# Performance work log

Hardware: AMD Instinct MI355X
Metric: run time of the kernel (lower is better)

The kernel has to match this reference:

```python
import jax, jax.numpy as jnp
import numpy as np
from jax import lax

H = 2048      # d_inner
N = 8         # half of d_state (conjugate-pair complex modes)
B, L, D_MODEL = 4, 4096, 1024
D_CONV = 4


def setup_inputs() -> dict:
    key = jax.random.key(0)
    ks = jax.random.split(key, 10)
    hidden_states = jax.random.normal(ks[0], (B, L, D_MODEL), dtype=jnp.float32)
    W_in = jax.random.normal(ks[1], (2 * H, D_MODEL), dtype=jnp.float32) / np.sqrt(D_MODEL)
    conv_w = jax.random.normal(ks[2], (H, D_CONV), dtype=jnp.float32) / np.sqrt(D_CONV)
    conv_b = jax.random.normal(ks[3], (H,), dtype=jnp.float32) * 0.1
    # S4D params: dt ~ loguniform(1e-3, 1e-1); A = -0.5 + i*pi*n (legs-ish diag init)
    u = jax.random.uniform(ks[4], (H,), dtype=jnp.float32)
    log_dt = jnp.log(1e-3) + u * (jnp.log(1e-1) - jnp.log(1e-3))
    log_A_real = jnp.log(0.5 * jnp.ones((H, N), dtype=jnp.float32))
    A_imag = jnp.pi * jnp.broadcast_to(jnp.arange(N, dtype=jnp.float32), (H, N)).copy()
    C_re = jax.random.normal(ks[5], (H, N), dtype=jnp.float32)
    C_im = jax.random.normal(ks[6], (H, N), dtype=jnp.float32)
    D = jnp.ones((H,), dtype=jnp.float32)
    W_out = jax.random.normal(ks[7], (D_MODEL, H), dtype=jnp.float32) / np.sqrt(H)
    return dict(hidden_states=hidden_states, W_in=W_in, conv_w=conv_w, conv_b=conv_b,
                log_dt=log_dt, log_A_real=log_A_real, A_imag=A_imag,
                C_re=C_re, C_im=C_im, D=D, W_out=W_out)


def _s4d_kernel(log_dt, log_A_real, A_imag, C_re, C_im, L):
    # S4D (diagonal SSM) convolution kernel, ZOH-style discretization.
    dt = jnp.exp(log_dt)                       # (H,)
    A = -jnp.exp(log_A_real) + 1j * A_imag      # (H,N) complex
    C = C_re + 1j * C_im                        # (H,N)
    dtA = dt[:, None] * A                       # (H,N)
    Ct = C * (jnp.exp(dtA) - 1.0) / A           # (H,N)
    t = jnp.arange(L, dtype=jnp.float32)
    vand = jnp.exp(dtA[:, :, None] * t)         # (H,N,L) Vandermonde
    return 2.0 * jnp.einsum('hn,hnl->hl', Ct, vand).real  # (H,L)


def reference(hidden_states, W_in, conv_w, conv_b, log_dt, log_A_real, A_imag, C_re, C_im, D, W_out):
    B, L, _ = hidden_states.shape
    # in_proj (no bias): (B,L,D) -> (B, 2H, L)
    xz = jnp.einsum('bld,ed->bel', hidden_states, W_in)
    x, z = jnp.split(xz, 2, axis=1)             # each (B,H,L)
    # causal depthwise conv1d + SiLU
    w = conv_w.shape[-1]
    xp = jnp.pad(x, ((0, 0), (0, 0), (w - 1, 0)))
    x = lax.conv_general_dilated(xp, conv_w[:, None, :], (1,), 'VALID',
                                 dimension_numbers=('NCH', 'OIH', 'NCH'),
                                 feature_group_count=x.shape[1])
    x = jax.nn.silu(x + conv_b[None, :, None])
    # S4 FFT long convolution + D skip
    k = _s4d_kernel(log_dt, log_A_real, A_imag, C_re, C_im, L)  # (H,L)
    n = 2 * L
    y = jnp.fft.irfft(jnp.fft.rfft(x, n=n) * jnp.fft.rfft(k, n=n), n=n)[..., :L]
    y = y + x * D[None, :, None]
    # SiLU gate and out_proj
    y = y * jax.nn.silu(z)
    return jnp.einsum('bhl,dh->bld', y, W_out)
```

## Files before the change

kernel.cpp:

```cpp
#include <hip/hip_runtime.h>
#include <hip/hip_bf16.h>
#include <math.h>

#define H_DIM 2048
#define N_ST 8
#define B_SZ 4
#define L_SEQ 4096
#define DMODEL 1024
#define DCONV 4
#define CL 128
#define NC (L_SEQ / CL)

typedef __bf16 bf16x8 __attribute__((ext_vector_type(8)));
typedef __bf16 bf16x4 __attribute__((ext_vector_type(4)));
typedef float f32x4 __attribute__((ext_vector_type(4)));

typedef const unsigned int __attribute__((address_space(1)))* gptr_t;
typedef unsigned int __attribute__((address_space(3)))* lptr_t;

__device__ __forceinline__ void gl_lds16(const __bf16* g, __bf16* l) {
    __builtin_amdgcn_global_load_lds((gptr_t)g, (lptr_t)l, 16, 0, 0);
}

#define WS_XZ     0
#define WS_YTH    8388608
#define WS_YTL    12582912
#define WS_COEF   16777216
#define WS_STATES 16875520
#define WS_LOOK   17924096
#define WS_HF     18186240
#define WS_WIF    24477696
#define WS_WOH    30769152
#define WS_WOL    31817728

__global__ __launch_bounds__(256) void cvt_split4(const float* __restrict__ s,
                                                  __bf16* __restrict__ h,
                                                  __bf16* __restrict__ l, int n4) {
    int i = blockIdx.x * 256 + threadIdx.x;
    if (i >= n4) return;
    float4 v = ((const float4*)s)[i];
    float vv[4] = {v.x, v.y, v.z, v.w};
    bf16x4 hv, lv;
#pragma unroll
    for (int j = 0; j < 4; ++j) {
        __bf16 hb = (__bf16)vv[j];
        hv[j] = hb;
        lv[j] = (__bf16)(vv[j] - (float)hb);
    }
    *(bf16x4*)&h[(size_t)i * 4] = hv;
    *(bf16x4*)&l[(size_t)i * 4] = lv;
}

template <int BSIDE>
__global__ __launch_bounds__(256) void cvt_fuse(const float* __restrict__ s,
                                                __bf16* __restrict__ d, int nOct) {
    int i = blockIdx.x * 256 + threadIdx.x;
    if (i >= nOct) return;
    int row = i >> 7, ko = i & 127;
    const float* p = s + (size_t)row * 1024 + ko * 8;
    float4 v0 = *(const float4*)p;
    float4 v1 = *(const float4*)(p + 4);
    float vv[8] = {v0.x, v0.y, v0.z, v0.w, v1.x, v1.y, v1.z, v1.w};
    bf16x8 hv, lv;
#pragma unroll
    for (int j = 0; j < 8; ++j) {
        __bf16 hb = (__bf16)vv[j];
        hv[j] = hb;
        lv[j] = (__bf16)(vv[j] - (float)hb);
    }
    __bf16* o = d + (size_t)row * 3072 + ko * 24;
    if (BSIDE) {
        *(bf16x8*)(o) = hv; *(bf16x8*)(o + 8) = lv; *(bf16x8*)(o + 16) = hv;
    } else {
        *(bf16x8*)(o) = hv; *(bf16x8*)(o + 8) = hv; *(bf16x8*)(o + 16) = lv;
    }
}

__global__ void coef_kernel(const float* __restrict__ log_dt,
                            const float* __restrict__ log_A_real,
                            const float* __restrict__ A_imag,
                            const float* __restrict__ C_re,
                            const float* __restrict__ C_im,
                            float* __restrict__ coef) {
    int i = blockIdx.x * blockDim.x + threadIdx.x;
    if (i >= H_DIM * N_ST) return;
    int h = i >> 3;
    float dt = expf(log_dt[h]);
    float Ar = -expf(log_A_real[i]);
    float Ai = A_imag[i];
    float er = expf(dt * Ar);
    float ang = dt * Ai;
    float wr = er * cosf(ang);
    float wi = er * sinf(ang);
    float den = Ar * Ar + Ai * Ai;
    float qr = ((wr - 1.f) * Ar + wi * Ai) / den;
    float qi = (wi * Ar - (wr - 1.f) * Ai) / den;
    float Cr = C_re[i], Ci = C_im[i];
    float Ctr = Cr * qr - Ci * qi;
    float Cti = Cr * qi + Ci * qr;
    float eCL = expf((float)CL * dt * Ar);
    float aCL = (float)CL * dt * Ai;
    float pr = eCL * cosf(aCL);
    float pi = eCL * sinf(aCL);
    const int HN = H_DIM * N_ST;
    coef[i]          = wr;
    coef[HN + i]     = wi;
    coef[2 * HN + i] = Ctr;
    coef[3 * HN + i] = Cti;
    coef[4 * HN + i] = pr;
    coef[5 * HN + i] = pi;
}

__global__ __launch_bounds__(512, 2) void gemm_f256p(const __bf16* __restrict__ A,
                                                     const __bf16* __restrict__ B,
                                                     float* __restrict__ C,
                                                     int K, int ldc) {
    __shared__ __bf16 sA[32768], sB[32768];
    const int tid = threadIdx.x;
    const int lane = tid & 63;
    const int wid = tid >> 6;
    const int wrw = wid >> 2, wcw = wid & 3;
    const int bm = blockIdx.y, bn = blockIdx.x;

    f32x4 acc[8][4];
#pragma unroll
    for (int m = 0; m < 8; ++m)
#pragma unroll
        for (int n = 0; n < 4; ++n) acc[m][n] = (f32x4){0.f, 0.f, 0.f, 0.f};

    const int kb = lane >> 4, rr = lane & 15;

    const int f0 = tid, f1 = 512 + tid;
    const int kA0 = f0 >> 8, rA0 = f0 & 255;
    const int kA1 = f1 >> 8, rA1 = f1 & 255;
    const size_t gA0 = (size_t)(bm * 256 + rA0) * K;
    const size_t gA1 = (size_t)(bm * 256 + rA1) * K;
    const size_t gB0 = (size_t)(bn * 256 + rA0) * K;
    const size_t gB1 = (size_t)(bn * 256 + rA1) * K;
    const int dst0 = kA0 * 2048 + rA0 * 8;
    const int dst1 = kA1 * 2048 + rA1 * 8;

    auto stageA = [&](int t, int ks) {
        const int base = (t & 1) * 16384 + ks * 8192;
        const size_t go = (size_t)t * 64 + ks * 32;
        gl_lds16(A + gA0 + go + kA0 * 8, &sA[base + dst0]);
        gl_lds16(A + gA1 + go + kA1 * 8, &sA[base + dst1]);
    };
    auto stageB = [&](int t, int ks) {
        const int base = (t & 1) * 16384 + ks * 8192;
        const size_t go = (size_t)t * 64 + ks * 32;
        gl_lds16(B + gB0 + go + kA0 * 8, &sB[base + dst0]);
        gl_lds16(B + gB1 + go + kA1 * 8, &sB[base + dst1]);
    };

    const int nt = K >> 6;
    stageA(0, 0); stageB(0, 0); stageA(0, 1); stageB(0, 1);
    asm volatile("s_waitcnt vmcnt(0)" ::: "memory");
    __builtin_amdgcn_s_barrier();
    __builtin_amdgcn_sched_barrier(0);

#pragma unroll 1
    for (int t = 0; t < nt; ++t) {
        const int par = (t & 1) * 16384;
        const bool pf = (t + 1 < nt);
        bf16x8 fB[4], fA[4];

        {
            const int bA = par, bB = par;
#pragma unroll
            for (int n = 0; n < 4; ++n)
                fB[n] = *(const bf16x8*)&sB[bB + kb * 2048 + (wcw * 64 + n * 16 + rr) * 8];
#pragma unroll
            for (int m = 0; m < 4; ++m)
                fA[m] = *(const bf16x8*)&sA[bA + kb * 2048 + (wrw * 128 + m * 16 + rr) * 8];
            if (pf) stageA(t + 1, 0);
            __builtin_amdgcn_s_barrier();
            asm volatile("s_waitcnt lgkmcnt(0)" ::: "memory");
            __builtin_amdgcn_sched_barrier(0);
            __builtin_amdgcn_s_setprio(1);
#pragma unroll
            for (int m = 0; m < 4; ++m)
#pragma unroll
                for (int n = 0; n < 4; ++n)
                    acc[m][n] = __builtin_amdgcn_mfma_f32_16x16x32_bf16(fA[m], fB[n], acc[m][n], 0, 0, 0);
            __builtin_amdgcn_s_setprio(0);
            __builtin_amdgcn_s_barrier();
            __builtin_amdgcn_sched_barrier(0);
        }
        {
            const int bA = par;
#pragma unroll
            for (int m = 0; m < 4; ++m)
                fA[m] = *(const bf16x8*)&sA[bA + kb * 2048 + (wrw * 128 + 64 + m * 16 + rr) * 8];
            if (pf) stageB(t + 1, 0);
            __builtin_amdgcn_s_barrier();
            asm volatile("s_waitcnt lgkmcnt(0)" ::: "memory");
            __builtin_amdgcn_sched_barrier(0);
            __builtin_amdgcn_s_setprio(1);
#pragma unroll
            for (int m = 0; m < 4; ++m)
#pragma unroll
                for (int n = 0; n < 4; ++n)
                    acc[4 + m][n] = __builtin_amdgcn_mfma_f32_16x16x32_bf16(fA[m], fB[n], acc[4 + m][n], 0, 0, 0);
            __builtin_amdgcn_s_setprio(0);
            if (pf) asm volatile("s_waitcnt vmcnt(4)" ::: "memory");
            else    asm volatile("s_waitcnt vmcnt(0)" ::: "memory");
            __builtin_amdgcn_s_barrier();
            __builtin_amdgcn_sched_barrier(0);
        }
        {
            const int bA = par + 8192, bB = par + 8192;
#pragma unroll
            for (int n = 0; n < 4; ++n)
                fB[n] = *(const bf16x8*)&sB[bB + kb * 2048 + (wcw * 64 + n * 16 + rr) * 8];
#pragma unroll
            for (int m = 0; m < 4; ++m)
                fA[m] = *(const bf16x8*)&sA[bA + kb * 2048 + (wrw * 128 + m * 16 + rr) * 8];
            if (pf) stageA(t + 1, 1);
            __builtin_amdgcn_s_barrier();
            asm volatile("s_waitcnt lgkmcnt(0)" ::: "memory");
            __builtin_amdgcn_sched_barrier(0);
            __builtin_amdgcn_s_setprio(1);
#pragma unroll
            for (int m = 0; m < 4; ++m)
#pragma unroll
                for (int n = 0; n < 4; ++n)
                    acc[m][n] = __builtin_amdgcn_mfma_f32_16x16x32_bf16(fA[m], fB[n], acc[m][n], 0, 0, 0);
            __builtin_amdgcn_s_setprio(0);
            __builtin_amdgcn_s_barrier();
            __builtin_amdgcn_sched_barrier(0);
        }
        {
            const int bA = par + 8192;
#pragma unroll
            for (int m = 0; m < 4; ++m)
                fA[m] = *(const bf16x8*)&sA[bA + kb * 2048 + (wrw * 128 + 64 + m * 16 + rr) * 8];
            if (pf) stageB(t + 1, 1);
            __builtin_amdgcn_s_barrier();
            asm volatile("s_waitcnt lgkmcnt(0)" ::: "memory");
            __builtin_amdgcn_sched_barrier(0);
            __builtin_amdgcn_s_setprio(1);
#pragma unroll
            for (int m = 0; m < 4; ++m)
#pragma unroll
                for (int n = 0; n < 4; ++n)
                    acc[4 + m][n] = __builtin_amdgcn_mfma_f32_16x16x32_bf16(fA[m], fB[n], acc[4 + m][n], 0, 0, 0);
            __builtin_amdgcn_s_setprio(0);
            if (pf) asm volatile("s_waitcnt vmcnt(4)" ::: "memory");
            else    asm volatile("s_waitcnt vmcnt(0)" ::: "memory");
            __builtin_amdgcn_s_barrier();
            __builtin_amdgcn_sched_barrier(0);
        }
    }

    const int rq = lane >> 4;
#pragma unroll
    for (int m = 0; m < 8; ++m)
#pragma unroll
        for (int n = 0; n < 4; ++n) {
            int col = bn * 256 + wcw * 64 + n * 16 + rr;
            int row0 = bm * 256 + wrw * 128 + m * 16 + rq * 4;
#pragma unroll
            for (int j = 0; j < 4; ++j)
                C[(size_t)(row0 + j) * ldc + col] = acc[m][n][j];
        }
}

__global__ __launch_bounds__(256, 1) void gemm_s128p(const __bf16* __restrict__ Ah,
                                                     const __bf16* __restrict__ Al,
                                                     const __bf16* __restrict__ Bh,
                                                     const __bf16* __restrict__ Bl,
                                                     float* __restrict__ C,
                                                     int K, int ldc) {
    __shared__ __bf16 sAh[2][2][4096], sAl[2][2][4096];
    __shared__ __bf16 sBh[2][2][4096], sBl[2][2][4096];
    const int tid = threadIdx.x;
    const int lane = tid & 63;
    const int wid = tid >> 6;
    const int wrw = wid >> 1, wcw = wid & 1;
    const int bm = blockIdx.y, bn = blockIdx.x;

    f32x4 acc[4][4];
#pragma unroll
    for (int m = 0; m < 4; ++m)
#pragma unroll
        for (int n = 0; n < 4; ++n) acc[m][n] = (f32x4){0.f, 0.f, 0.f, 0.f};

    const int kb = lane >> 4, rr = lane & 15;

    const int fl0 = tid, fl1 = 256 + tid;
    const int kbs0 = fl0 >> 7, rw0 = fl0 & 127;
    const int kbs1 = fl1 >> 7, rw1 = fl1 & 127;
    const size_t gAr0 = (size_t)(bm * 128 + rw0) * K;
    const size_t gAr1 = (size_t)(bm * 128 + rw1) * K;
    const size_t gBr0 = (size_t)(bn * 128 + rw0) * K;
    const size_t gBr1 = (size_t)(bn * 128 + rw1) * K;
    const int d0 = kbs0 * 1024 + rw0 * 8;
    const int d1 = kbs1 * 1024 + rw1 * 8;

    auto stA = [&](int t, int ks) {
        const int par = t & 1;
        const size_t go = (size_t)t * 64 + ks * 32;
        gl_lds16(Ah + gAr0 + go + kbs0 * 8, &sAh[par][ks][d0]);
        gl_lds16(Ah + gAr1 + go + kbs1 * 8, &sAh[par][ks][d1]);
        gl_lds16(Al + gAr0 + go + kbs0 * 8, &sAl[par][ks][d0]);
        gl_lds16(Al + gAr1 + go + kbs1 * 8, &sAl[par][ks][d1]);
    };
    auto stB = [&](int t, int ks) {
        const int par = t & 1;
        const size_t go = (size_t)t * 64 + ks * 32;
        gl_lds16(Bh + gBr0 + go + kbs0 * 8, &sBh[par][ks][d0]);
        gl_lds16(Bh + gBr1 + go + kbs1 * 8, &sBh[par][ks][d1]);
        gl_lds16(Bl + gBr0 + go + kbs0 * 8, &sBl[par][ks][d0]);
        gl_lds16(Bl + gBr1 + go + kbs1 * 8, &sBl[par][ks][d1]);
    };

    const int nt = K >> 6;
    stA(0, 0); stB(0, 0); stA(0, 1); stB(0, 1);
    asm volatile("s_waitcnt vmcnt(0)" ::: "memory");
    __builtin_amdgcn_s_barrier();
    __builtin_amdgcn_sched_barrier(0);

    bf16x8 fAh[4], fAl[4], fBh[4], fBl[4];

#pragma unroll 1
    for (int t = 0; t < nt; ++t) {
        const int par = t & 1;
        const bool pf = (t + 1 < nt);

        {
#pragma unroll
            for (int n = 0; n < 4; ++n) {
                const int off = kb * 1024 + (wcw * 64 + n * 16 + rr) * 8;
                fBh[n] = *(const bf16x8*)&sBh[par][0][off];
                fBl[n] = *(const bf16x8*)&sBl[par][0][off];
            }
#pragma unroll
            for (int m = 0; m < 4; ++m) {
                const int off = kb * 1024 + (wrw * 64 + m * 16 + rr) * 8;
                fAh[m] = *(const bf16x8*)&sAh[par][0][off];
                fAl[m] = *(const bf16x8*)&sAl[par][0][off];
            }
            if (pf) stA(t + 1, 0);
            __builtin_amdgcn_s_barrier();
            asm volatile("s_waitcnt lgkmcnt(0)" ::: "memory");
            __builtin_amdgcn_sched_barrier(0);
            __builtin_amdgcn_s_setprio(1);
#pragma unroll
            for (int m = 0; m < 2; ++m)
#pragma unroll
                for (int n = 0; n < 4; ++n) {
                    acc[m][n] = __builtin_amdgcn_mfma_f32_16x16x32_bf16(fAh[m], fBh[n], acc[m][n], 0, 0, 0);
                    acc[m][n] = __builtin_amdgcn_mfma_f32_16x16x32_bf16(fAh[m], fBl[n], acc[m][n], 0, 0, 0);
                    acc[m][n] = __builtin_amdgcn_mfma_f32_16x16x32_bf16(fAl[m], fBh[n], acc[m][n], 0, 0, 0);
                }
            __builtin_amdgcn_s_setprio(0);
            __builtin_amdgcn_s_barrier();
            __builtin_amdgcn_sched_barrier(0);
        }
        {
            if (pf) stB(t + 1, 0);
            __builtin_amdgcn_s_barrier();
            __builtin_amdgcn_sched_barrier(0);
            __builtin_amdgcn_s_setprio(1);
#pragma unroll
            for (int m = 2; m < 4; ++m)
#pragma unroll
                for (int n = 0; n < 4; ++n) {
                    acc[m][n] = __builtin_amdgcn_mfma_f32_16x16x32_bf16(fAh[m], fBh[n], acc[m][n], 0, 0, 0);
                    acc[m][n] = __builtin_amdgcn_mfma_f32_16x16x32_bf16(fAh[m], fBl[n], acc[m][n], 0, 0, 0);
                    acc[m][n] = __builtin_amdgcn_mfma_f32_16x16x32_bf16(fAl[m], fBh[n], acc[m][n], 0, 0, 0);
                }
            __builtin_amdgcn_s_setprio(0);
            if (pf) asm volatile("s_waitcnt vmcnt(8)" ::: "memory");
            else    asm volatile("s_waitcnt vmcnt(0)" ::: "memory");
            __builtin_amdgcn_s_barrier();
            __builtin_amdgcn_sched_barrier(0);
        }
        {
#pragma unroll
            for (int n = 0; n < 4; ++n) {
                const int off = kb * 1024 + (wcw * 64 + n * 16 + rr) * 8;
                fBh[n] = *(const bf16x8*)&sBh[par][1][off];
                fBl[n] = *(const bf16x8*)&sBl[par][1][off];
            }
#pragma unroll
            for (int m = 0; m < 4; ++m) {
                const int off = kb * 1024 + (wrw * 64 + m * 16 + rr) * 8;
                fAh[m] = *(const bf16x8*)&sAh[par][1][off];
                fAl[m] = *(const bf16x8*)&sAl[par][1][off];
            }
            if (pf) stA(t + 1, 1);
            __builtin_amdgcn_s_barrier();
            asm volatile("s_waitcnt lgkmcnt(0)" ::: "memory");
            __builtin_amdgcn_sched_barrier(0);
            __builtin_amdgcn_s_setprio(1);
#pragma unroll
            for (int m = 0; m < 2; ++m)
#pragma unroll
                for (int n = 0; n < 4; ++n) {
                    acc[m][n] = __builtin_amdgcn_mfma_f32_16x16x32_bf16(fAh[m], fBh[n], acc[m][n], 0, 0, 0);
                    acc[m][n] = __builtin_amdgcn_mfma_f32_16x16x32_bf16(fAh[m], fBl[n], acc[m][n], 0, 0, 0);
                    acc[m][n] = __builtin_amdgcn_mfma_f32_16x16x32_bf16(fAl[m], fBh[n], acc[m][n], 0, 0, 0);
                }
            __builtin_amdgcn_s_setprio(0);
            __builtin_amdgcn_s_barrier();
            __builtin_amdgcn_sched_barrier(0);
        }
        {
            if (pf) stB(t + 1, 1);
            __builtin_amdgcn_s_barrier();
            __builtin_amdgcn_sched_barrier(0);
            __builtin_amdgcn_s_setprio(1);
#pragma unroll
            for (int m = 2; m < 4; ++m)
#pragma unroll
                for (int n = 0; n < 4; ++n) {
                    acc[m][n] = __builtin_amdgcn_mfma_f32_16x16x32_bf16(fAh[m], fBh[n], acc[m][n], 0, 0, 0);
                    acc[m][n] = __builtin_amdgcn_mfma_f32_16x16x32_bf16(fAh[m], fBl[n], acc[m][n], 0, 0, 0);
                    acc[m][n] = __builtin_amdgcn_mfma_f32_16x16x32_bf16(fAl[m], fBh[n], acc[m][n], 0, 0, 0);
                }
            __builtin_amdgcn_s_setprio(0);
            if (pf) asm volatile("s_waitcnt vmcnt(8)" ::: "memory");
            else    asm volatile("s_waitcnt vmcnt(0)" ::: "memory");
            __builtin_amdgcn_s_barrier();
            __builtin_amdgcn_sched_barrier(0);
        }
    }

    const int rq = lane >> 4;
#pragma unroll
    for (int m = 0; m < 4; ++m)
#pragma unroll
        for (int n = 0; n < 4; ++n) {
            int col = bn * 128 + wcw * 64 + n * 16 + rr;
            int row0 = bm * 128 + wrw * 64 + m * 16 + rq * 4;
#pragma unroll
            for (int j = 0; j < 4; ++j)
                C[(size_t)(row0 + j) * ldc + col] = acc[m][n][j];
        }
}

__global__ __launch_bounds__(256) void scan_phase1(const float* __restrict__ xz,
                                                   const float* __restrict__ coef,
                                                   const float* __restrict__ conv_w,
                                                   const float* __restrict__ conv_b,
                                                   float* __restrict__ states,
                                                   float* __restrict__ look) {
    int t = blockIdx.x * 256 + threadIdx.x;
    int c = t & (NC - 1);
    int h = t >> 5;

    const int HN = H_DIM * N_ST;
    float wr[N_ST], wi[N_ST];
#pragma unroll
    for (int n = 0; n < N_ST; ++n) {
        wr[n] = coef[h * N_ST + n];
        wi[n] = coef[HN + h * N_ST + n];
    }
    float cw0 = conv_w[h * 4 + 0], cw1 = conv_w[h * 4 + 1];
    float cw2 = conv_w[h * 4 + 2], cw3 = conv_w[h * 4 + 3];
    float cb = conv_b[h];

    const float* xrow = xz + (size_t)h * L_SEQ + c * CL;
    float x3 = 0.f, x2 = 0.f, x1 = 0.f;
    if (c > 0) {
        float4 p = *(const float4*)(xrow - 4);
        x3 = p.y; x2 = p.z; x1 = p.w;
    }
    *(float4*)(look + (size_t)t * 4) = make_float4(x3, x2, x1, 0.f);

    float sr[N_ST], si[N_ST];
#pragma unroll
    for (int n = 0; n < N_ST; ++n) { sr[n] = 0.f; si[n] = 0.f; }

    for (int j = 0; j < CL; j += 4) {
        float4 v = *(const float4*)(xrow + j);
        float xv[4] = {v.x, v.y, v.z, v.w};
#pragma unroll
        for (int k = 0; k < 4; ++k) {
            float u = cw0 * x3 + cw1 * x2 + cw2 * x1 + cw3 * xv[k] + cb;
            float xc = u / (1.f + __expf(-u));
            x3 = x2; x2 = x1; x1 = xv[k];
#pragma unroll
            for (int n = 0; n < N_ST; ++n) {
                float nr = wr[n] * sr[n] - wi[n] * si[n] + xc;
                float ni = wr[n] * si[n] + wi[n] * sr[n];
                sr[n] = nr; si[n] = ni;
            }
        }
    }
    float* st = states + (size_t)t * (N_ST * 2);
#pragma unroll
    for (int n = 0; n < N_ST; ++n) { st[2 * n] = sr[n]; st[2 * n + 1] = si[n]; }
}

__global__ __launch_bounds__(256) void scan_phase2(const float* __restrict__ coef,
                                                   float* __restrict__ states) {
    int h = blockIdx.x * 256 + threadIdx.x;
    if (h >= H_DIM) return;
    const int HN = H_DIM * N_ST;
    float pr[N_ST], pi[N_ST];
#pragma unroll
    for (int n = 0; n < N_ST; ++n) {
        pr[n] = coef[4 * HN + h * N_ST + n];
        pi[n] = coef[5 * HN + h * N_ST + n];
    }
    float sr[N_ST], si[N_ST];
#pragma unroll
    for (int n = 0; n < N_ST; ++n) { sr[n] = 0.f; si[n] = 0.f; }
    float* base = states + (size_t)h * NC * (N_ST * 2);
    for (int c = 0; c < NC; ++c) {
        float* st = base + c * (N_ST * 2);
#pragma unroll
        for (int n = 0; n < N_ST; ++n) {
            float lr = st[2 * n], li = st[2 * n + 1];
            st[2 * n] = sr[n]; st[2 * n + 1] = si[n];
            float nr = pr[n] * sr[n] - pi[n] * si[n] + lr;
            float ni = pr[n] * si[n] + pi[n] * sr[n] + li;
            sr[n] = nr; si[n] = ni;
        }
    }
}

__global__ __launch_bounds__(256) void scan_phase3(float* __restrict__ xz,
                                                   const float* __restrict__ coef,
                                                   const float* __restrict__ conv_w,
                                                   const float* __restrict__ conv_b,
                                                   const float* __restrict__ Dvec,
                                                   const float* __restrict__ states,
                                                   const float* __restrict__ look) {
    int t = blockIdx.x * 256 + threadIdx.x;
    int c = t & (NC - 1);
    int h = t >> 5;

    const int HN = H_DIM * N_ST;
    float wr[N_ST], wi[N_ST], Ctr[N_ST], Cti[N_ST];
#pragma unroll
    for (int n = 0; n < N_ST; ++n) {
        wr[n]  = coef[h * N_ST + n];
        wi[n]  = coef[HN + h * N_ST + n];
        Ctr[n] = coef[2 * HN + h * N_ST + n];
        Cti[n] = coef[3 * HN + h * N_ST + n];
    }
    float cw0 = conv_w[h * 4 + 0], cw1 = conv_w[h * 4 + 1];
    float cw2 = conv_w[h * 4 + 2], cw3 = conv_w[h * 4 + 3];
    float cb = conv_b[h];
    float Dh = Dvec[h];

    float* xrow = xz + (size_t)h * L_SEQ + c * CL;
    const float* zrow = xz + (size_t)(H_DIM + h) * L_SEQ + c * CL;

    float4 lk = *(const float4*)(look + (size_t)t * 4);
    float x3 = lk.x, x2 = lk.y, x1 = lk.z;

    const float* st = states + (size_t)t * (N_ST * 2);
    float sr[N_ST], si[N_ST];
#pragma unroll
    for (int n = 0; n < N_ST; ++n) { sr[n] = st[2 * n]; si[n] = st[2 * n + 1]; }

    for (int j = 0; j < CL; j += 4) {
        float4 v = *(const float4*)(xrow + j);
        float4 zv = *(const float4*)(zrow + j);
        float xv[4] = {v.x, v.y, v.z, v.w};
        float zz[4] = {zv.x, zv.y, zv.z, zv.w};
        float out[4];
#pragma unroll
        for (int k = 0; k < 4; ++k) {
            float u = cw0 * x3 + cw1 * x2 + cw2 * x1 + cw3 * xv[k] + cb;
            float xc = u / (1.f + __expf(-u));
            x3 = x2; x2 = x1; x1 = xv[k];
            float accy = 0.f;
#pragma unroll
            for (int n = 0; n < N_ST; ++n) {
                float nr = wr[n] * sr[n] - wi[n] * si[n] + xc;
                float ni = wr[n] * si[n] + wi[n] * sr[n];
                sr[n] = nr; si[n] = ni;
                accy += Ctr[n] * nr - Cti[n] * ni;
            }
            float yv = 2.f * accy + Dh * xc;
            float g = zz[k] / (1.f + __expf(-zz[k]));
            out[k] = yv * g;
        }
        *(float4*)(xrow + j) = make_float4(out[0], out[1], out[2], out[3]);
    }
}

__global__ __launch_bounds__(256) void transpose_split(const float* __restrict__ y,
                                                       __bf16* __restrict__ th,
                                                       __bf16* __restrict__ tl) {
    __shared__ float tile[64][65];
    const int l0 = blockIdx.x * 64, h0 = blockIdx.y * 64;
    const int tid = threadIdx.x;
    const int r = tid >> 4, c4 = (tid & 15) * 4;
#pragma unroll
    for (int p = 0; p < 4; ++p) {
        float4 v = *(const float4*)(y + (size_t)(h0 + r + p * 16) * L_SEQ + l0 + c4);
        tile[r + p * 16][c4 + 0] = v.x;
        tile[r + p * 16][c4 + 1] = v.y;
        tile[r + p * 16][c4 + 2] = v.z;
        tile[r + p * 16][c4 + 3] = v.w;
    }
    __syncthreads();
    const int l = tid >> 2, hb = (tid & 3) * 16;
    float vals[16];
#pragma unroll
    for (int j = 0; j < 16; ++j) vals[j] = tile[hb + j][l];
    bf16x8 hv0, hv1, lv0, lv1;
#pragma unroll
    for (int j = 0; j < 8; ++j) {
        __bf16 hbv = (__bf16)vals[j];
        hv0[j] = hbv;
        lv0[j] = (__bf16)(vals[j] - (float)hbv);
        __bf16 hbv2 = (__bf16)vals[j + 8];
        hv1[j] = hbv2;
        lv1[j] = (__bf16)(vals[j + 8] - (float)hbv2);
    }
    size_t base = (size_t)(l0 + l) * H_DIM + h0 + hb;
    *(bf16x8*)&th[base] = hv0;
    *(bf16x8*)&th[base + 8] = hv1;
    *(bf16x8*)&tl[base] = lv0;
    *(bf16x8*)&tl[base + 8] = lv1;
}

extern "C" void kernel_launch(void* const* d_in, const int* in_sizes, int n_in,
                              void* d_out, int out_size, void* d_ws, size_t ws_size,
                              hipStream_t stream) {
    const float* hid        = (const float*)d_in[0];
    const float* W_in       = (const float*)d_in[1];
    const float* conv_w     = (const float*)d_in[2];
    const float* conv_b     = (const float*)d_in[3];
    const float* log_dt     = (const float*)d_in[4];
    const float* log_A_real = (const float*)d_in[5];
    const float* A_imag     = (const float*)d_in[6];
    const float* C_re       = (const float*)d_in[7];
    const float* C_im       = (const float*)d_in[8];
    const float* Dv         = (const float*)d_in[9];
    const float* W_out      = (const float*)d_in[10];
    float* out = (float*)d_out;
    float* ws  = (float*)d_ws;

    float* xz      = ws + WS_XZ;
    __bf16* yTh    = (__bf16*)(ws + WS_YTH);
    __bf16* yTl    = (__bf16*)(ws + WS_YTL);
    float* coef    = ws + WS_COEF;
    float* states  = ws + WS_STATES;
    float* look    = ws + WS_LOOK;
    __bf16* Hf     = (__bf16*)(ws + WS_HF);
    __bf16* WiF    = (__bf16*)(ws + WS_WIF);
    __bf16* Woh    = (__bf16*)(ws + WS_WOH);
    __bf16* Wol    = (__bf16*)(ws + WS_WOL);

    coef_kernel<<<(H_DIM * N_ST + 255) / 256, 256, 0, stream>>>(
        log_dt, log_A_real, A_imag, C_re, C_im, coef);

    const int wOct = 2 * H_DIM * DMODEL / 8;
    cvt_fuse<0><<<(wOct + 255) / 256, 256, 0, stream>>>(W_in, WiF, wOct);
    cvt_split4<<<(DMODEL * H_DIM / 4 + 255) / 256, 256, 0, stream>>>(W_out, Woh, Wol, DMODEL * H_DIM / 4);

    const int nscan = H_DIM * NC;
    const int hOct = L_SEQ * DMODEL / 8;
    dim3 gIn(L_SEQ / 256, 2 * H_DIM / 256);
    dim3 gOut(DMODEL / 128, L_SEQ / 128);
    dim3 gTr(L_SEQ / 64, H_DIM / 64);

    for (int b = 0; b < B_SZ; ++b) {
        const float* hid_b = hid + (size_t)b * L_SEQ * DMODEL;
        float* out_b = out + (size_t)b * L_SEQ * DMODEL;

        cvt_fuse<1><<<(hOct + 255) / 256, 256, 0, stream>>>(hid_b, Hf, hOct);
        gemm_f256p<<<gIn, 512, 0, stream>>>(WiF, Hf, xz, 3 * DMODEL, L_SEQ);
        scan_phase1<<<nscan / 256, 256, 0, stream>>>(xz, coef, conv_w, conv_b, states, look);
        scan_phase2<<<(H_DIM + 255) / 256, 256, 0, stream>>>(coef, states);
        scan_phase3<<<nscan / 256, 256, 0, stream>>>(xz, coef, conv_w, conv_b, Dv, states, look);
        transpose_split<<<gTr, 256, 0, stream>>>(xz, yTh, yTl);
        gemm_s128p<<<gOut, 256, 0, stream>>>(yTh, yTl, Woh, Wol, out_b, H_DIM, DMODEL);
    }
}
```

Baseline: 1.467 ms.

## Double-buffer LDS fragment reads in registers to overlap with MFMA in both GEMMs

Restructures the main loops of both GEMM kernels so that LDS-to-register fragment reads for the next MFMA phase are issued before the current phase's MFMAs run. Ping-pong register fragment sets replace the single set, and the explicit lgkmcnt(0) waits before each MFMA block are dropped. This also removes one barrier per phase. The aim is to hide LDS read latency and barrier stalls behind matrix math, at the cost of more VGPRs. It relies on the compiler inserting correct lgkm waits, and the reduced barriers carry some risk of LDS read/write races on the double buffer.

```diff
diff --git a/kernel.cpp b/kernel.cpp
--- a/kernel.cpp
+++ b/kernel.cpp
@@ -153,104 +153,98 @@
         gl_lds16(B + gB1 + go + kA1 * 8, &sB[base + dst1]);
     };
 
+    bf16x8 fB0[4], fB1[4];
+    bf16x8 fA0[4], fA1[4];
+
+    auto readB = [&](bf16x8* dst, int base) {
+#pragma unroll
+        for (int n = 0; n < 4; ++n)
+            dst[n] = *(const bf16x8*)&sB[base + kb * 2048 + (wcw * 64 + n * 16 + rr) * 8];
+    };
+    auto readA = [&](bf16x8* dst, int base, int mh) {
+#pragma unroll
+        for (int m = 0; m < 4; ++m)
+            dst[m] = *(const bf16x8*)&sA[base + kb * 2048 + (wrw * 128 + mh * 64 + m * 16 + rr) * 8];
+    };
+
     const int nt = K >> 6;
     stageA(0, 0); stageB(0, 0); stageA(0, 1); stageB(0, 1);
     asm volatile("s_waitcnt vmcnt(0)" ::: "memory");
     __builtin_amdgcn_s_barrier();
     __builtin_amdgcn_sched_barrier(0);
+    readB(fB0, 0);
+    readA(fA0, 0, 0);
+    __builtin_amdgcn_sched_barrier(0);
 
 #pragma unroll 1
     for (int t = 0; t < nt; ++t) {
         const int par = (t & 1) * 16384;
+        const int parn = ((t + 1) & 1) * 16384;
         const bool pf = (t + 1 < nt);
-        bf16x8 fB[4], fA[4];
-
-        {
-            const int bA = par, bB = par;
+
+        if (pf) stageA(t + 1, 0);
+        __builtin_amdgcn_s_barrier();
+        __builtin_amdgcn_sched_barrier(0);
+        readA(fA1, par, 1);
+        __builtin_amdgcn_sched_barrier(0);
+        __builtin_amdgcn_s_setprio(1);
+#pragma unroll
+        for (int m = 0; m < 4; ++m)
 #pragma unroll
             for (int n = 0; n < 4; ++n)
-                fB[n] = *(const bf16x8*)&sB[bB + kb * 2048 + (wcw * 64 + n * 16 + rr) * 8];
-#pragma unroll
-            for (int m = 0; m < 4; ++m)
-                fA[m] = *(const bf16x8*)&sA[bA + kb * 2048 + (wrw * 128 + m * 16 + rr) * 8];
-            if (pf) stageA(t + 1, 0);
-            __builtin_amdgcn_s_barrier();
-            asm volatile("s_waitcnt lgkmcnt(0)" ::: "memory");
-            __builtin_amdgcn_sched_barrier(0);
-            __builtin_amdgcn_s_setprio(1);
-#pragma unroll
-            for (int m = 0; m < 4; ++m)
-#pragma unroll
-                for (int n = 0; n < 4; ++n)
-                    acc[m][n] = __builtin_amdgcn_mfma_f32_16x16x32_bf16(fA[m], fB[n], acc[m][n], 0, 0, 0);
-            __builtin_amdgcn_s_setprio(0);
-            __builtin_amdgcn_s_barrier();
-            __builtin_amdgcn_sched_barrier(0);
-        }
-        {
-            const int bA = par;
-#pragma unroll
-            for (int m = 0; m < 4; ++m)
-                fA[m] = *(const bf16x8*)&sA[bA + kb * 2048 + (wrw * 128 + 64 + m * 16 + rr) * 8];
-            if (pf) stageB(t + 1, 0);
-            __builtin_amdgcn_s_barrier();
-            asm volatile("s_waitcnt lgkmcnt(0)" ::: "memory");
-            __builtin_amdgcn_sched_barrier(0);
-            __builtin_amdgcn_s_setprio(1);
-#pragma unroll
-            for (int m = 0; m < 4; ++m)
-#pragma unroll
-                for (int n = 0; n < 4; ++n)
-                    acc[4 + m][n] = __builtin_amdgcn_mfma_f32_16x16x32_bf16(fA[m], fB[n], acc[4 + m][n], 0, 0, 0);
-            __builtin_amdgcn_s_setprio(0);
-            if (pf) asm volatile("s_waitcnt vmcnt(4)" ::: "memory");
-            else    asm volatile("s_waitcnt vmcnt(0)" ::: "memory");
-            __builtin_amdgcn_s_barrier();
-            __builtin_amdgcn_sched_barrier(0);
-        }
-        {
-            const int bA = par + 8192, bB = par + 8192;
+                acc[m][n] = __builtin_amdgcn_mfma_f32_16x16x32_bf16(fA0[m], fB0[n], acc[m][n], 0, 0, 0);
+        __builtin_amdgcn_s_setprio(0);
+        __builtin_amdgcn_sched_barrier(0);
+
+        if (pf) stageB(t + 1, 0);
+        if (pf) asm volatile("s_waitcnt vmcnt(4)" ::: "memory");
+        else    asm volatile("s_waitcnt vmcnt(0)" ::: "memory");
+        __builtin_amdgcn_s_barrier();
+        __builtin_amdgcn_sched_barrier(0);
+        readB(fB1, par + 8192);
+        readA(fA0, par + 8192, 0);
+        __builtin_amdgcn_sched_barrier(0);
+        __builtin_amdgcn_s_setprio(1);
+#pragma unroll
+        for (int m = 0; m < 4; ++m)
 #pragma unroll
             for (int n = 0; n < 4; ++n)
-                fB[n] = *(const bf16x8*)&sB[bB + kb * 2048 + (wcw * 64 + n * 16 + rr) * 8];
-#pragma unroll
-            for (int m = 0; m < 4; ++m)
-                fA[m] = *(const bf16x8*)&sA[bA + kb * 2048 + (wrw * 128 + m * 16 + rr) * 8];
-            if (pf) stageA(t + 1, 1);
-            __builtin_amdgcn_s_barrier();
-            asm volatile("s_waitcnt lgkmcnt(0)" ::: "memory");
-            __builtin_amdgcn_sched_barrier(0);
-            __builtin_amdgcn_s_setprio(1);
-#pragma unroll
-            for (int m = 0; m < 4; ++m)
-#pragma unroll
-                for (int n = 0; n < 4; ++n)
-                    acc[m][n] = __builtin_amdgcn_mfma_f32_16x16x32_bf16(fA[m], fB[n], acc[m][n], 0, 0, 0);
-            __builtin_amdgcn_s_setprio(0);
-            __builtin_amdgcn_s_barrier();
-            __builtin_amdgcn_sched_barrier(0);
-        }
-        {
-            const int bA = par + 8192;
-#pragma unroll
-            for (int m = 0; m < 4; ++m)
-                fA[m] = *(const bf16x8*)&sA[bA + kb * 2048 + (wrw * 128 + 64 + m * 16 + rr) * 8];
-            if (pf) stageB(t + 1, 1);
-            __builtin_amdgcn_s_barrier();
-            asm volatile("s_waitcnt lgkmcnt(0)" ::: "memory");
-            __builtin_amdgcn_sched_barrier(0);
-            __builtin_amdgcn_s_setprio(1);
-#pragma unroll
-            for (int m = 0; m < 4; ++m)
-#pragma unroll
-                for (int n = 0; n < 4; ++n)
-                    acc[4 + m][n] = __builtin_amdgcn_mfma_f32_16x16x32_bf16(fA[m], fB[n], acc[4 + m][n], 0, 0, 0);
-            __builtin_amdgcn_s_setprio(0);
-            if (pf) asm volatile("s_waitcnt vmcnt(4)" ::: "memory");
-            else    asm volatile("s_waitcnt vmcnt(0)" ::: "memory");
-            __builtin_amdgcn_s_barrier();
-            __builtin_amdgcn_sched_barrier(0);
-        }
+                acc[4 + m][n] = __builtin_amdgcn_mfma_f32_16x16x32_bf16(fA1[m], fB0[n], acc[4 + m][n], 0, 0, 0);
+        __builtin_amdgcn_s_setprio(0);
+        __builtin_amdgcn_sched_barrier(0);
+
+        if (pf) stageA(t + 1, 1);
+        __builtin_amdgcn_s_barrier();
+        __builtin_amdgcn_sched_barrier(0);
+        readA(fA1, par + 8192, 1);
+        __builtin_amdgcn_sched_barrier(0);
+        __builtin_amdgcn_s_setprio(1);
+#pragma unroll
+        for (int m = 0; m < 4; ++m)
+#pragma unroll
+            for (int n = 0; n < 4; ++n)
+                acc[m][n] = __builtin_amdgcn_mfma_f32_16x16x32_bf16(fA0[m], fB1[n], acc[m][n], 0, 0, 0);
+        __builtin_amdgcn_s_setprio(0);
+        __builtin_amdgcn_sched_barrier(0);
+
+        if (pf) stageB(t + 1, 1);
+        if (pf) asm volatile("s_waitcnt vmcnt(4)" ::: "memory");
+        else    asm volatile("s_waitcnt vmcnt(0)" ::: "memory");
+        __builtin_amdgcn_s_barrier();
+        __builtin_amdgcn_sched_barrier(0);
+        if (pf) {
+            readB(fB0, parn);
+            readA(fA0, parn, 0);
+        }
+        __builtin_amdgcn_sched_barrier(0);
+        __builtin_amdgcn_s_setprio(1);
+#pragma unroll
+        for (int m = 0; m < 4; ++m)
+#pragma unroll
+            for (int n = 0; n < 4; ++n)
+                acc[4 + m][n] = __builtin_amdgcn_mfma_f32_16x16x32_bf16(fA1[m], fB1[n], acc[4 + m][n], 0, 0, 0);
+        __builtin_amdgcn_s_setprio(0);
+        __builtin_amdgcn_sched_barrier(0);
     }
 
     const int rq = lane >> 4;
@@ -315,117 +309,116 @@
         gl_lds16(Bl + gBr1 + go + kbs1 * 8, &sBl[par][ks][d1]);
     };
 
+    bf16x8 fBh0[4], fBl0[4], fBh1[4], fBl1[4];
+    bf16x8 fAh0[2], fAl0[2], fAh1[2], fAl1[2];
+
+    auto readB = [&](bf16x8* dh, bf16x8* dl, int par, int ks) {
+#pragma unroll
+        for (int n = 0; n < 4; ++n) {
+            const int off = kb * 1024 + (wcw * 64 + n * 16 + rr) * 8;
+            dh[n] = *(const bf16x8*)&sBh[par][ks][off];
+            dl[n] = *(const bf16x8*)&sBl[par][ks][off];
+        }
+    };
+    auto readA2 = [&](bf16x8* dh, bf16x8* dl, int par, int ks, int mlo) {
+#pragma unroll
+        for (int m = 0; m < 2; ++m) {
+            const int off = kb * 1024 + (wrw * 64 + (mlo + m) * 16 + rr) * 8;
+            dh[m] = *(const bf16x8*)&sAh[par][ks][off];
+            dl[m] = *(const bf16x8*)&sAl[par][ks][off];
+        }
+    };
+
     const int nt = K >> 6;
     stA(0, 0); stB(0, 0); stA(0, 1); stB(0, 1);
     asm volatile("s_waitcnt vmcnt(0)" ::: "memory");
     __builtin_amdgcn_s_barrier();
     __builtin_amdgcn_sched_barrier(0);
-
-    bf16x8 fAh[4], fAl[4], fBh[4], fBl[4];
+    readB(fBh0, fBl0, 0, 0);
+    readA2(fAh0, fAl0, 0, 0, 0);
+    __builtin_amdgcn_sched_barrier(0);
 
 #pragma unroll 1
     for (int t = 0; t < nt; ++t) {
         const int par = t & 1;
+        const int parn = (t + 1) & 1;
         const bool pf = (t + 1 < nt);
 
-        {
+        if (pf) stA(t + 1, 0);
+        __builtin_amdgcn_s_barrier();
+        __builtin_amdgcn_sched_barrier(0);
+        readA2(fAh1, fAl1, par, 0, 2);
+        __builtin_amdgcn_sched_barrier(0);
+        __builtin_amdgcn_s_setprio(1);
+#pragma unroll
+        for (int m = 0; m < 2; ++m)
 #pragma unroll
             for (int n = 0; n < 4; ++n) {
-                const int off = kb * 1024 + (wcw * 64 + n * 16 + rr) * 8;
-                fBh[n] = *(const bf16x8*)&sBh[par][0][off];
-                fBl[n] = *(const bf16x8*)&sBl[par][0][off];
+                acc[m][n] = __builtin_amdgcn_mfma_f32_16x16x32_bf16(fAh0[m], fBh0[n], acc[m][n], 0, 0, 0);
+                acc[m][n] = __builtin_amdgcn_mfma_f32_16x16x32_bf16(fAh0[m], fBl0[n], acc[m][n], 0, 0, 0);
+                acc[m][n] = __builtin_amdgcn_mfma_f32_16x16x32_bf16(fAl0[m], fBh0[n], acc[m][n], 0, 0, 0);
             }
-#pragma unroll
-            for (int m = 0; m < 4; ++m) {
-                const int off = kb * 1024 + (wrw * 64 + m * 16 + rr) * 8;
-                fAh[m] = *(const bf16x8*)&sAh[par][0][off];
-                fAl[m] = *(const bf16x8*)&sAl[par][0][off];
+        __builtin_amdgcn_s_setprio(0);
+        __builtin_amdgcn_sched_barrier(0);
+
+        if (pf) stB(t + 1, 0);
+        if (pf) asm volatile("s_waitcnt vmcnt(8)" ::: "memory");
+        else    asm volatile("s_waitcnt vmcnt(0)" ::: "memory");
+        __builtin_amdgcn_s_barrier();
+        __builtin_amdgcn_sched_barrier(0);
+        readB(fBh1, fBl1, par, 1);
+        readA2(fAh0, fAl0, par, 1, 0);
+        __builtin_amdgcn_sched_barrier(0);
+        __builtin_amdgcn_s_setprio(1);
+#pragma unroll
+        for (int m = 0; m < 2; ++m)
+#pragma unroll
+            for (int n = 0; n < 4; ++n) {
+                acc[2 + m][n] = __builtin_amdgcn_mfma_f32_16x16x32_bf16(fAh1[m], fBh0[n], acc[2 + m][n], 0, 0, 0);
+                acc[2 + m][n] = __builtin_amdgcn_mfma_f32_16x16x32_bf16(fAh1[m], fBl0[n], acc[2 + m][n], 0, 0, 0);
+                acc[2 + m][n] = __builtin_amdgcn_mfma_f32_16x16x32_bf16(fAl1[m], fBh0[n], acc[2 + m][n], 0, 0, 0);
             }
-            if (pf) stA(t + 1, 0);
-            __builtin_amdgcn_s_barrier();
-            asm volatile("s_waitcnt lgkmcnt(0)" ::: "memory");
-            __builtin_amdgcn_sched_barrier(0);
-            __builtin_amdgcn_s_setprio(1);
-#pragma unroll
-            for (int m = 0; m < 2; ++m)
-#pragma unroll
-                for (int n = 0; n < 4; ++n) {
-                    acc[m][n] = __builtin_amdgcn_mfma_f32_16x16x32_bf16(fAh[m], fBh[n], acc[m][n], 0, 0, 0);
-                    acc[m][n] = __builtin_amdgcn_mfma_f32_16x16x32_bf16(fAh[m], fBl[n], acc[m][n], 0, 0, 0);
-                    acc[m][n] = __builtin_amdgcn_mfma_f32_16x16x32_bf16(fAl[m], fBh[n], acc[m][n], 0, 0, 0);
-                }
-            __builtin_amdgcn_s_setprio(0);
-            __builtin_amdgcn_s_barrier();
-            __builtin_amdgcn_sched_barrier(0);
-        }
-        {
-            if (pf) stB(t + 1, 0);
-            __builtin_amdgcn_s_barrier();
-            __builtin_amdgcn_sched_barrier(0);
-            __builtin_amdgcn_s_setprio(1);
-#pragma unroll
-            for (int m = 2; m < 4; ++m)
-#pragma unroll
-                for (int n = 0; n < 4; ++n) {
-                    acc[m][n] = __builtin_amdgcn_mfma_f32_16x16x32_bf16(fAh[m], fBh[n], acc[m][n], 0, 0, 0);
-                    acc[m][n] = __builtin_amdgcn_mfma_f32_16x16x32_bf16(fAh[m], fBl[n], acc[m][n], 0, 0, 0);
-                    acc[m][n] = __builtin_amdgcn_mfma_f32_16x16x32_bf16(fAl[m], fBh[n], acc[m][n], 0, 0, 0);
-                }
-            __builtin_amdgcn_s_setprio(0);
-            if (pf) asm volatile("s_waitcnt vmcnt(8)" ::: "memory");
-            else    asm volatile("s_waitcnt vmcnt(0)" ::: "memory");
-            __builtin_amdgcn_s_barrier();
-            __builtin_amdgcn_sched_barrier(0);
-        }
-        {
+        __builtin_amdgcn_s_setprio(0);
+        __builtin_amdgcn_sched_barrier(0);
+
+        if (pf) stA(t + 1, 1);
+        __builtin_amdgcn_s_barrier();
+        __builtin_amdgcn_sched_barrier(0);
+        readA2(fAh1, fAl1, par, 1, 2);
+        __builtin_amdgcn_sched_barrier(0);
+        __builtin_amdgcn_s_setprio(1);
+#pragma unroll
+        for (int m = 0; m < 2; ++m)
 #pragma unroll
             for (int n = 0; n < 4; ++n) {
-                const int off = kb * 1024 + (wcw * 64 + n * 16 + rr) * 8;
-                fBh[n] = *(const bf16x8*)&sBh[par][1][off];
-                fBl[n] = *(const bf16x8*)&sBl[par][1][off];
+                acc[m][n] = __builtin_amdgcn_mfma_f32_16x16x32_bf16(fAh0[m], fBh1[n], acc[m][n], 0, 0, 0);
+                acc[m][n] = __builtin_amdgcn_mfma_f32_16x16x32_bf16(fAh0[m], fBl1[n], acc[m][n], 0, 0, 0);
+                acc[m][n] = __builtin_amdgcn_mfma_f32_16x16x32_bf16(fAl0[m], fBh1[n], acc[m][n], 0, 0, 0);
             }
-#pragma unroll
-            for (int m = 0; m < 4; ++m) {
-                const int off = kb * 1024 + (wrw * 64 + m * 16 + rr) * 8;
-                fAh[m] = *(const bf16x8*)&sAh[par][1][off];
-                fAl[m] = *(const bf16x8*)&sAl[par][1][off];
+        __builtin_amdgcn_s_setprio(0);
+        __builtin_amdgcn_sched_barrier(0);
+
+        if (pf) stB(t + 1, 1);
+        if (pf) asm volatile("s_waitcnt vmcnt(8)" ::: "memory");
+        else    asm volatile("s_waitcnt vmcnt(0)" ::: "memory");
+        __builtin_amdgcn_s_barrier();
+        __builtin_amdgcn_sched_barrier(0);
+        if (pf) {
+            readB(fBh0, fBl0, parn, 0);
+            readA2(fAh0, fAl0, parn, 0, 0);
+        }
+        __builtin_amdgcn_sched_barrier(0);
+        __builtin_amdgcn_s_setprio(1);
+#pragma unroll
+        for (int m = 0; m < 2; ++m)
+#pragma unroll
+            for (int n = 0; n < 4; ++n) {
+                acc[2 + m][n] = __builtin_amdgcn_mfma_f32_16x16x32_bf16(fAh1[m], fBh1[n], acc[2 + m][n], 0, 0, 0);
+                acc[2 + m][n] = __builtin_amdgcn_mfma_f32_16x16x32_bf16(fAh1[m], fBl1[n], acc[2 + m][n], 0, 0, 0);
+                acc[2 + m][n] = __builtin_amdgcn_mfma_f32_16x16x32_bf16(fAl1[m], fBh1[n], acc[2 + m][n], 0, 0, 0);
             }
-            if (pf) stA(t + 1, 1);
-            __builtin_amdgcn_s_barrier();
-            asm volatile("s_waitcnt lgkmcnt(0)" ::: "memory");
-            __builtin_amdgcn_sched_barrier(0);
-            __builtin_amdgcn_s_setprio(1);
-#pragma unroll
-            for (int m = 0; m < 2; ++m)
-#pragma unroll
-                for (int n = 0; n < 4; ++n) {
-                    acc[m][n] = __builtin_amdgcn_mfma_f32_16x16x32_bf16(fAh[m], fBh[n], acc[m][n], 0, 0, 0);
-                    acc[m][n] = __builtin_amdgcn_mfma_f32_16x16x32_bf16(fAh[m], fBl[n], acc[m][n], 0, 0, 0);
-                    acc[m][n] = __builtin_amdgcn_mfma_f32_16x16x32_bf16(fAl[m], fBh[n], acc[m][n], 0, 0, 0);
-                }
-            __builtin_amdgcn_s_setprio(0);
-            __builtin_amdgcn_s_barrier();
-            __builtin_amdgcn_sched_barrier(0);
-        }
-        {
-            if (pf) stB(t + 1, 1);
-            __builtin_amdgcn_s_barrier();
-            __builtin_amdgcn_sched_barrier(0);
-            __builtin_amdgcn_s_setprio(1);
-#pragma unroll
-            for (int m = 2; m < 4; ++m)
-#pragma unroll
-                for (int n = 0; n < 4; ++n) {
-                    acc[m][n] = __builtin_amdgcn_mfma_f32_16x16x32_bf16(fAh[m], fBh[n], acc[m][n], 0, 0, 0);
-                    acc[m][n] = __builtin_amdgcn_mfma_f32_16x16x32_bf16(fAh[m], fBl[n], acc[m][n], 0, 0, 0);
-                    acc[m][n] = __builtin_amdgcn_mfma_f32_16x16x32_bf16(fAl[m], fBh[n], acc[m][n], 0, 0, 0);
-                }
-            __builtin_amdgcn_s_setprio(0);
-            if (pf) asm volatile("s_waitcnt vmcnt(8)" ::: "memory");
-            else    asm volatile("s_waitcnt vmcnt(0)" ::: "memory");
-            __builtin_amdgcn_s_barrier();
-            __builtin_amdgcn_sched_barrier(0);
-        }
+        __builtin_amdgcn_s_setprio(0);
+        __builtin_amdgcn_sched_barrier(0);
     }
 
     const int rq = lane >> 4;
```

New measurement: 1.567 ms. 6.8% more time.

## Run in-proj GEMM with 1024-thread blocks, halving per-wave tile

Applied to the files above, without the earlier changes.

The 256x256 in-projection GEMM moves from 8 waves per block to 16 waves per block. Each wave now computes a 64x64 sub-tile instead of 128x64, so it holds half as many accumulators, and each thread issues one async global-to-LDS load per stage instead of two. The intent is more waves per CU to hide latency and lower register pressure per wave. In exchange, launch bounds drop to 1 block per CU, and each wave does less MFMA work between barriers, so the four-phase barrier schedule costs relatively more.

```diff
diff --git a/kernel.cpp b/kernel.cpp
--- a/kernel.cpp
+++ b/kernel.cpp
@@ -111,10 +111,10 @@
     coef[5 * HN + i] = pi;
 }
 
-__global__ __launch_bounds__(512, 2) void gemm_f256p(const __bf16* __restrict__ A,
-                                                     const __bf16* __restrict__ B,
-                                                     float* __restrict__ C,
-                                                     int K, int ldc) {
+__global__ __launch_bounds__(1024, 1) void gemm_f256w(const __bf16* __restrict__ A,
+                                                      const __bf16* __restrict__ B,
+                                                      float* __restrict__ C,
+                                                      int K, int ldc) {
     __shared__ __bf16 sA[32768], sB[32768];
     const int tid = threadIdx.x;
     const int lane = tid & 63;
@@ -122,35 +122,28 @@
     const int wrw = wid >> 2, wcw = wid & 3;
     const int bm = blockIdx.y, bn = blockIdx.x;
 
-    f32x4 acc[8][4];
-#pragma unroll
-    for (int m = 0; m < 8; ++m)
+    f32x4 acc[4][4];
+#pragma unroll
+    for (int m = 0; m < 4; ++m)
 #pragma unroll
         for (int n = 0; n < 4; ++n) acc[m][n] = (f32x4){0.f, 0.f, 0.f, 0.f};
 
     const int kb = lane >> 4, rr = lane & 15;
 
-    const int f0 = tid, f1 = 512 + tid;
-    const int kA0 = f0 >> 8, rA0 = f0 & 255;
-    const int kA1 = f1 >> 8, rA1 = f1 & 255;
+    const int kA0 = tid >> 8, rA0 = tid & 255;
     const size_t gA0 = (size_t)(bm * 256 + rA0) * K;
-    const size_t gA1 = (size_t)(bm * 256 + rA1) * K;
     const size_t gB0 = (size_t)(bn * 256 + rA0) * K;
-    const size_t gB1 = (size_t)(bn * 256 + rA1) * K;
     const int dst0 = kA0 * 2048 + rA0 * 8;
-    const int dst1 = kA1 * 2048 + rA1 * 8;
 
     auto stageA = [&](int t, int ks) {
         const int base = (t & 1) * 16384 + ks * 8192;
-        const size_t go = (size_t)t * 64 + ks * 32;
-        gl_lds16(A + gA0 + go + kA0 * 8, &sA[base + dst0]);
-        gl_lds16(A + gA1 + go + kA1 * 8, &sA[base + dst1]);
+        const size_t go = (size_t)t * 64 + ks * 32 + kA0 * 8;
+        gl_lds16(A + gA0 + go, &sA[base + dst0]);
     };
     auto stageB = [&](int t, int ks) {
         const int base = (t & 1) * 16384 + ks * 8192;
-        const size_t go = (size_t)t * 64 + ks * 32;
-        gl_lds16(B + gB0 + go + kA0 * 8, &sB[base + dst0]);
-        gl_lds16(B + gB1 + go + kA1 * 8, &sB[base + dst1]);
+        const size_t go = (size_t)t * 64 + ks * 32 + kA0 * 8;
+        gl_lds16(B + gB0 + go, &sB[base + dst0]);
     };
 
     const int nt = K >> 6;
@@ -166,20 +159,19 @@
         bf16x8 fB[4], fA[4];
 
         {
-            const int bA = par, bB = par;
 #pragma unroll
             for (int n = 0; n < 4; ++n)
-                fB[n] = *(const bf16x8*)&sB[bB + kb * 2048 + (wcw * 64 + n * 16 + rr) * 8];
-#pragma unroll
-            for (int m = 0; m < 4; ++m)
-                fA[m] = *(const bf16x8*)&sA[bA + kb * 2048 + (wrw * 128 + m * 16 + rr) * 8];
+                fB[n] = *(const bf16x8*)&sB[par + kb * 2048 + (wcw * 64 + n * 16 + rr) * 8];
+#pragma unroll
+            for (int m = 0; m < 2; ++m)
+                fA[m] = *(const bf16x8*)&sA[par + kb * 2048 + (wrw * 64 + m * 16 + rr) * 8];
             if (pf) stageA(t + 1, 0);
             __builtin_amdgcn_s_barrier();
             asm volatile("s_waitcnt lgkmcnt(0)" ::: "memory");
             __builtin_amdgcn_sched_barrier(0);
             __builtin_amdgcn_s_setprio(1);
 #pragma unroll
-            for (int m = 0; m < 4; ++m)
+            for (int m = 0; m < 2; ++m)
 #pragma unroll
                 for (int n = 0; n < 4; ++n)
                     acc[m][n] = __builtin_amdgcn_mfma_f32_16x16x32_bf16(fA[m], fB[n], acc[m][n], 0, 0, 0);
@@ -188,65 +180,64 @@
             __builtin_amdgcn_sched_barrier(0);
         }
         {
-            const int bA = par;
-#pragma unroll
-            for (int m = 0; m < 4; ++m)
-                fA[m] = *(const bf16x8*)&sA[bA + kb * 2048 + (wrw * 128 + 64 + m * 16 + rr) * 8];
+#pragma unroll
+            for (int m = 2; m < 4; ++m)
+                fA[m] = *(const bf16x8*)&sA[par + kb * 2048 + (wrw * 64 + m * 16 + rr) * 8];
             if (pf) stageB(t + 1, 0);
             __builtin_amdgcn_s_barrier();
             asm volatile("s_waitcnt lgkmcnt(0)" ::: "memory");
             __builtin_amdgcn_sched_barrier(0);
             __builtin_amdgcn_s_setprio(1);
 #pragma unroll
-            for (int m = 0; m < 4; ++m)
-#pragma unroll
-                for (int n = 0; n < 4; ++n)
-                    acc[4 + m][n] = __builtin_amdgcn_mfma_f32_16x16x32_bf16(fA[m], fB[n], acc[4 + m][n], 0, 0, 0);
-            __builtin_amdgcn_s_setprio(0);
-            if (pf) asm volatile("s_waitcnt vmcnt(4)" ::: "memory");
-            else    asm volatile("s_waitcnt vmcnt(0)" ::: "memory");
-            __builtin_amdgcn_s_barrier();
-            __builtin_amdgcn_sched_barrier(0);
-        }
-        {
-            const int bA = par + 8192, bB = par + 8192;
-#pragma unroll
-            for (int n = 0; n < 4; ++n)
-                fB[n] = *(const bf16x8*)&sB[bB + kb * 2048 + (wcw * 64 + n * 16 + rr) * 8];
-#pragma unroll
-            for (int m = 0; m < 4; ++m)
-                fA[m] = *(const bf16x8*)&sA[bA + kb * 2048 + (wrw * 128 + m * 16 + rr) * 8];
-            if (pf) stageA(t + 1, 1);
-            __builtin_amdgcn_s_barrier();
-            asm volatile("s_waitcnt lgkmcnt(0)" ::: "memory");
-            __builtin_amdgcn_sched_barrier(0);
-            __builtin_amdgcn_s_setprio(1);
-#pragma unroll
-            for (int m = 0; m < 4; ++m)
+            for (int m = 2; m < 4; ++m)
 #pragma unroll
                 for (int n = 0; n < 4; ++n)
                     acc[m][n] = __builtin_amdgcn_mfma_f32_16x16x32_bf16(fA[m], fB[n], acc[m][n], 0, 0, 0);
             __builtin_amdgcn_s_setprio(0);
-            __builtin_amdgcn_s_barrier();
-            __builtin_amdgcn_sched_barrier(0);
-        }
-        {
-            const int bA = par + 8192;
-#pragma unroll
-            for (int m = 0; m < 4; ++m)
-                fA[m] = *(const bf16x8*)&sA[bA + kb * 2048 + (wrw * 128 + 64 + m * 16 + rr) * 8];
+            if (pf) asm volatile("s_waitcnt vmcnt(2)" ::: "memory");
+            else    asm volatile("s_waitcnt vmcnt(0)" ::: "memory");
+            __builtin_amdgcn_s_barrier();
+            __builtin_amdgcn_sched_barrier(0);
+        }
+        {
+            const int b1 = par + 8192;
+#pragma unroll
+            for (int n = 0; n < 4; ++n)
+                fB[n] = *(const bf16x8*)&sB[b1 + kb * 2048 + (wcw * 64 + n * 16 + rr) * 8];
+#pragma unroll
+            for (int m = 0; m < 2; ++m)
+                fA[m] = *(const bf16x8*)&sA[b1 + kb * 2048 + (wrw * 64 + m * 16 + rr) * 8];
+            if (pf) stageA(t + 1, 1);
+            __builtin_amdgcn_s_barrier();
+            asm volatile("s_waitcnt lgkmcnt(0)" ::: "memory");
+            __builtin_amdgcn_sched_barrier(0);
+            __builtin_amdgcn_s_setprio(1);
+#pragma unroll
+            for (int m = 0; m < 2; ++m)
+#pragma unroll
+                for (int n = 0; n < 4; ++n)
+                    acc[m][n] = __builtin_amdgcn_mfma_f32_16x16x32_bf16(fA[m], fB[n], acc[m][n], 0, 0, 0);
+            __builtin_amdgcn_s_setprio(0);
+            __builtin_amdgcn_s_barrier();
+            __builtin_amdgcn_sched_barrier(0);
+        }
+        {
+            const int b1 = par + 8192;
+#pragma unroll
+            for (int m = 2; m < 4; ++m)
+                fA[m] = *(const bf16x8*)&sA[b1 + kb * 2048 + (wrw * 64 + m * 16 + rr) * 8];
             if (pf) stageB(t + 1, 1);
             __builtin_amdgcn_s_barrier();
             asm volatile("s_waitcnt lgkmcnt(0)" ::: "memory");
             __builtin_amdgcn_sched_barrier(0);
             __builtin_amdgcn_s_setprio(1);
 #pragma unroll
-            for (int m = 0; m < 4; ++m)
+            for (int m = 2; m < 4; ++m)
 #pragma unroll
                 for (int n = 0; n < 4; ++n)
-                    acc[4 + m][n] = __builtin_amdgcn_mfma_f32_16x16x32_bf16(fA[m], fB[n], acc[4 + m][n], 0, 0, 0);
-            __builtin_amdgcn_s_setprio(0);
-            if (pf) asm volatile("s_waitcnt vmcnt(4)" ::: "memory");
+                    acc[m][n] = __builtin_amdgcn_mfma_f32_16x16x32_bf16(fA[m], fB[n], acc[m][n], 0, 0, 0);
+            __builtin_amdgcn_s_setprio(0);
+            if (pf) asm volatile("s_waitcnt vmcnt(2)" ::: "memory");
             else    asm volatile("s_waitcnt vmcnt(0)" ::: "memory");
             __builtin_amdgcn_s_barrier();
             __builtin_amdgcn_sched_barrier(0);
@@ -255,11 +246,11 @@
 
     const int rq = lane >> 4;
 #pragma unroll
-    for (int m = 0; m < 8; ++m)
+    for (int m = 0; m < 4; ++m)
 #pragma unroll
         for (int n = 0; n < 4; ++n) {
             int col = bn * 256 + wcw * 64 + n * 16 + rr;
-            int row0 = bm * 256 + wrw * 128 + m * 16 + rq * 4;
+            int row0 = bm * 256 + wrw * 64 + m * 16 + rq * 4;
 #pragma unroll
             for (int j = 0; j < 4; ++j)
                 C[(size_t)(row0 + j) * ldc + col] = acc[m][n][j];
@@ -669,7 +660,7 @@
         float* out_b = out + (size_t)b * L_SEQ * DMODEL;
 
         cvt_fuse<1><<<(hOct + 255) / 256, 256, 0, stream>>>(hid_b, Hf, hOct);
-        gemm_f256p<<<gIn, 512, 0, stream>>>(WiF, Hf, xz, 3 * DMODEL, L_SEQ);
+        gemm_f256w<<<gIn, 1024, 0, stream>>>(WiF, Hf, xz, 3 * DMODEL, L_SEQ);
         scan_phase1<<<nscan / 256, 256, 0, stream>>>(xz, coef, conv_w, conv_b, states, look);
         scan_phase2<<<(H_DIM + 255) / 256, 256, 0, stream>>>(coef, states);
         scan_phase3<<<nscan / 256, 256, 0, stream>>>(xz, coef, conv_w, conv_b, Dv, states, look);
```

Result: slower. 1.559 ms (+6.3%).
